# Performance work log

Measured on AMD Instinct MI355X. Metric: run time of the kernel, lower is better.

The kernel has to match this reference:

```python
import jax, jax.numpy as jnp
import numpy as np

KEY_SIZE = 256
EPS = 1e-8  # torch F.cosine_similarity default eps


def setup_inputs() -> dict:
    key = jax.random.key(0)
    k1, k2 = jax.random.split(key)
    B, M, K, V = 2048, 100000, KEY_SIZE, 256
    query = jax.random.normal(k1, (B, K), dtype=jnp.float32)
    memory = jax.random.normal(k2, (M, K + V), dtype=jnp.float32)
    return {"query": query, "memory": memory}


def reference(query, memory):
    # memory: [M, K+V] -> keys [M, K], values [M, V]
    keys = memory[:, :KEY_SIZE]
    values = memory[:, KEY_SIZE:]
    # cosine similarity: (q . k) / max(|q|*|k|, eps)  -> [B, M]
    dots = jnp.einsum('bk,mk->bm', query, keys)
    qn = jnp.linalg.norm(query, axis=1)  # [B]
    kn = jnp.linalg.norm(keys, axis=1)   # [M]
    sims = dots / jnp.maximum(qn[:, None] * kn[None, :], EPS)
    # top-1 over memory dim, then gather values -> [B, V]
    idx = jnp.argmax(sims, axis=1)
    return values[idx]
```

## Files before the change

kernel.cpp:

```cpp
#include <hip/hip_runtime.h>
#include <hip/hip_fp16.h>
#include <float.h>

#define MKEY 256
#define NMEM 100000
#define NPAD 100096
#define NQ   2048
#define BM 128
#define BN 128
#define NTILES 782
#define BLKPAD 800
#define GRID (128 * 98)
#define KEYBLOCKS (NPAD / 4)
#define QS (127.0f / 6.0f)
#define SS2 ((6.0f / 127.0f) * (6.0f / 127.0f))
#define GDELTA 0.04f
#define GINVD  25.0f

typedef int i32x4 __attribute__((ext_vector_type(4)));

__device__ inline void gll16(const void* g, void* l) {
  __builtin_amdgcn_global_load_lds(
      (const __attribute__((address_space(1))) unsigned*)g,
      (__attribute__((address_space(3))) unsigned*)l, 16, 0, 0);
}

__device__ inline int pack_i8x4(float4 v) {
  int c0 = max(-127, min(127, __float2int_rn(v.x * QS)));
  int c1 = max(-127, min(127, __float2int_rn(v.y * QS)));
  int c2 = max(-127, min(127, __float2int_rn(v.z * QS)));
  int c3 = max(-127, min(127, __float2int_rn(v.w * QS)));
  return (c0 & 255) | ((c1 & 255) << 8) | ((c2 & 255) << 16) | ((c3 & 255) << 24);
}

__device__ inline int dot4i8(int a, int b, int s) {
#if __has_builtin(__builtin_amdgcn_sdot4)
  return __builtin_amdgcn_sdot4(a, b, s, false);
#else
#pragma unroll
  for (int k = 0; k < 4; ++k) {
    const int av = (a << (24 - 8 * k)) >> 24;
    const int bv = (b << (24 - 8 * k)) >> 24;
    s += av * bv;
  }
  return s;
#endif
}

__global__ void convert(const float* __restrict__ q, const float* __restrict__ mem,
                        int* __restrict__ qi, int* __restrict__ ki,
                        float* __restrict__ rkn) {
  const int b = blockIdx.x;
  if (b >= KEYBLOCKS) {
    const int i = (b - KEYBLOCKS) * 256 + threadIdx.x;
    const float4 v = *(const float4*)&q[(size_t)i * 4];
    qi[i] = pack_i8x4(v);
    return;
  }
  const int t = threadIdx.x, lane = t & 63, w = t >> 6;
  const int row = b * 4 + w;
  if (row < NMEM) {
    const float4 v = *(const float4*)&mem[(long)row * 512 + lane * 4];
    const float ss0 = v.x * v.x + v.y * v.y + v.z * v.z + v.w * v.w;
    ki[(size_t)row * 64 + lane] = pack_i8x4(v);
    float ss = ss0;
#pragma unroll
    for (int off = 32; off >= 1; off >>= 1) ss += __shfl_xor(ss, off, 64);
    if (lane == 0) rkn[row] = 1.0f / sqrtf(fmaxf(ss, 1e-30f));
  } else {
    ki[(size_t)row * 64 + lane] = 0;
    if (lane == 0) rkn[row] = 0.f;
  }
}

__global__ __launch_bounds__(256, 4) void gemm_screen(
    const int* __restrict__ qi, const int* __restrict__ ki,
    const float* __restrict__ rkn,
    unsigned long long* __restrict__ bcode8, float* __restrict__ bmaxB) {
  __shared__ __align__(128) char smem[33792];

  const int id = blockIdx.x;
  const int mtile = (id >> 3) & 15;
  const int ntile = (id & 7) + 8 * (id >> 7);
  if (ntile >= NTILES) return;

  const int t = threadIdx.x;
  const int w = t >> 6;
  const int lane = t & 63;
  const int wr = w >> 1, wc = w & 1;
  const int q16 = lane >> 4, l16 = lane & 15;

  const int swz64 = ((lane & 3) ^ ((lane >> 2) & 3)) * 16;
  int soff4[4];
#pragma unroll
  for (int c = 0; c < 4; ++c)
    soff4[c] = ((w & 1) * 64 + c * 16 + (lane >> 2)) * 256 + swz64;
  const char* const asrc = (const char*)((w < 2) ? qi : ki) +
                           (size_t)(((w < 2) ? mtile : ntile) * 128) * 256;
  char* const dbase = smem + ((w < 2) ? 0 : 16384) + (w & 1) * 4096;

#define STG(p, s)                                         \
  do {                                                    \
    const char* _s = asrc + (s) * 64;                     \
    char* _d = dbase + (p) * 8192;                        \
    _Pragma("unroll")                                     \
    for (int c = 0; c < 4; ++c)                           \
      gll16(_s + soff4[c], _d + c * 1024);                \
  } while (0)

  i32x4 acc[4][4];
#pragma unroll
  for (int i = 0; i < 4; i++)
#pragma unroll
    for (int j = 0; j < 4; j++) acc[i][j] = (i32x4){0, 0, 0, 0};

  const int pc4 = (q16 ^ (l16 & 3)) * 16;

  STG(0, 0);
  __syncthreads();
#pragma unroll
  for (int s = 0; s < 4; ++s) {
    if (s < 3) STG((s + 1) & 1, s + 1);
    const int p = (s & 1) * 8192;
    i32x4 av[4], bv[4];
#pragma unroll
    for (int i = 0; i < 4; i++)
      av[i] = *(const i32x4*)&smem[p + (64 * wr + 16 * i + l16) * 64 + pc4];
#pragma unroll
    for (int j = 0; j < 4; j++)
      bv[j] = *(const i32x4*)&smem[16384 + p + (64 * wc + 16 * j + l16) * 64 + pc4];
#pragma unroll
    for (int i = 0; i < 4; i++)
#pragma unroll
      for (int j = 0; j < 4; j++)
        acc[i][j] = __builtin_amdgcn_mfma_i32_16x16x64_i8(av[i], bv[j], acc[i][j], 0, 0, 0);
    __syncthreads();
  }
#undef STG

  float rk[4];
#pragma unroll
  for (int j = 0; j < 4; j++) {
    const int ncol = ntile * BN + 64 * wc + 16 * j + l16;
    rk[j] = (ncol < NMEM) ? rkn[ncol] * SS2 : 0.f;
  }
  float (*L)[20] = (float(*)[20])smem;
  float* bhalf = (float*)(smem + 32768);
  const int wr_ = t >> 7, gg = (t >> 4) & 7, qrow = t & 15;
  float outv[4];
#pragma unroll
  for (int i = 0; i < 4; ++i) {
#pragma unroll
    for (int j = 0; j < 4; ++j)
#pragma unroll
      for (int r = 0; r < 4; ++r)
        L[(wr * 8 + wc * 4 + j) * 16 + q16 * 4 + r][l16] = (float)acc[i][j][r] * rk[j];
    __syncthreads();
    const float* Lr = L[(wr_ * 8 + gg) * 16 + qrow];
    const float4 a = *(const float4*)&Lr[0], b4 = *(const float4*)&Lr[4];
    const float4 cc = *(const float4*)&Lr[8], dd = *(const float4*)&Lr[12];
    float m = fmaxf(fmaxf(fmaxf(a.x, a.y), fmaxf(a.z, a.w)),
                    fmaxf(fmaxf(b4.x, b4.y), fmaxf(b4.z, b4.w)));
    m = fmaxf(m, fmaxf(fmaxf(cc.x, cc.y), fmaxf(cc.z, cc.w)));
    m = fmaxf(m, fmaxf(fmaxf(dd.x, dd.y), fmaxf(dd.z, dd.w)));
    outv[i] = m;
    float bm = fmaxf(m, __shfl_xor(m, 16, 64));
    bm = fmaxf(bm, __shfl_xor(bm, 32, 64));
    if (lane < 16) bhalf[(w * 16 + lane) * 4 + i] = bm;
    __syncthreads();
  }
  float* brow = (float*)smem;
  unsigned char* cb = (unsigned char*)(smem + 512);
  if (t < 128) {
    const int wrb = t >> 6, ib = (t >> 4) & 3, qr = t & 15;
    const float v = fmaxf(bhalf[((2 * wrb) * 16 + qr) * 4 + ib],
                          bhalf[((2 * wrb + 1) * 16 + qr) * 4 + ib]);
    brow[t] = v;
    bmaxB[(size_t)ntile * NQ + mtile * 128 + t] = v;
  }
  __syncthreads();
#pragma unroll
  for (int i = 0; i < 4; ++i) {
    const int row = wr_ * 64 + i * 16 + qrow;
    int code = (int)((brow[row] - outv[i]) * GINVD);
    code = min(255, max(0, code));
    cb[row * 8 + gg] = (unsigned char)code;
  }
  __syncthreads();
  if (t < 128)
    bcode8[(size_t)ntile * NQ + mtile * 128 + t] =
        *(const unsigned long long*)&cb[t * 8];
}

__global__ __launch_bounds__(256) void transpose_blk(const float* __restrict__ in,
                                                     float* __restrict__ outp) {
  __shared__ float tl[32][33];
  const int bid = blockIdx.x;
  const int ntt = bid % 25, qt = bid / 25;
  const int r0 = ntt * 32, c0 = qt * 32;
  const int tx = threadIdx.x & 31, ty = threadIdx.x >> 5;
#pragma unroll
  for (int k = 0; k < 4; ++k) {
    const int r = r0 + ty + 8 * k;
    tl[ty + 8 * k][tx] = (r < NTILES) ? in[(size_t)r * NQ + c0 + tx] : -FLT_MAX;
  }
  __syncthreads();
#pragma unroll
  for (int k = 0; k < 4; ++k) {
    const int qq = c0 + ty + 8 * k;
    const int nt = r0 + tx;
    if (nt < NTILES) outp[(size_t)qq * BLKPAD + nt] = tl[tx][ty + 8 * k];
  }
}

__global__ __launch_bounds__(256) void rescore_gather(
    const float* __restrict__ q, const float* __restrict__ mem,
    const int* __restrict__ qi8, const int* __restrict__ ki8,
    const float* __restrict__ rkn, const float* __restrict__ bmaxQ,
    const unsigned long long* __restrict__ bcode8, float* __restrict__ out) {
  __shared__ float red2[4];
  __shared__ int blist[64];
  __shared__ int nblk;
  __shared__ int glist[128];
  __shared__ int ng;
  __shared__ int rlist[256];
  __shared__ int nrow;
  __shared__ double wb[4];
  __shared__ int wbi[4];
  __shared__ int widx;

  const int qid = blockIdx.x;
  const int t = threadIdx.x, w = t >> 6, lane = t & 63;

  const float4 qv = *(const float4*)&q[(size_t)qid * 256 + lane * 4];
  float ss = qv.x * qv.x + qv.y * qv.y + qv.z * qv.z + qv.w * qv.w;
#pragma unroll
  for (int off = 32; off >= 1; off >>= 1) ss += __shfl_xor(ss, off, 64);
  const float qn = sqrtf(ss);
  const float margin = 1.8e-2f * qn;

  int4 qreg[4];
#pragma unroll
  for (int k = 0; k < 4; ++k)
    qreg[k] = *(const int4*)&qi8[(size_t)qid * 64 + (lane & 3) * 16 + k * 4];

  if (t == 0) { nblk = 0; ng = 0; nrow = 0; }
  const float* bq = &bmaxQ[(size_t)qid * BLKPAD];

  float gm = -FLT_MAX;
  for (int i = t; i < NTILES; i += 256) gm = fmaxf(gm, bq[i]);
#pragma unroll
  for (int off = 32; off >= 1; off >>= 1) gm = fmaxf(gm, __shfl_xor(gm, off, 64));
  if (lane == 0) red2[w] = gm;
  __syncthreads();
  gm = fmaxf(fmaxf(red2[0], red2[1]), fmaxf(red2[2], red2[3]));
  const float thresh = gm - margin;

  for (int i = t; i < NTILES; i += 256)
    if (bq[i] >= thresh) {
      int p = atomicAdd(&nblk, 1);
      if (p < 64) blist[p] = i;
    }
  __syncthreads();
  const int nb_ = min(nblk, 64);

  for (int idx = t; idx < nb_ * 8; idx += 256) {
    const int nt = blist[idx >> 3], gl = idx & 7;
    const unsigned long long cw = bcode8[(size_t)nt * NQ + qid];
    const int code = (int)((cw >> (8 * gl)) & 255);
    if ((float)code * GDELTA <= bq[nt] - thresh + 1e-6f) {
      int p = atomicAdd(&ng, 1);
      if (p < 128) glist[p] = nt * 8 + gl;
    }
  }
  __syncthreads();
  const int ng_ = min(ng, 128);

  for (int c = w; c < ng_; c += 4) {
    const int row = glist[c] * 16 + (lane >> 2);
    int idot = 0;
#pragma unroll
    for (int k = 0; k < 4; ++k) {
      const int4 kv = *(const int4*)&ki8[(size_t)row * 64 + (lane & 3) * 16 + k * 4];
      idot = dot4i8(kv.x, qreg[k].x, idot);
      idot = dot4i8(kv.y, qreg[k].y, idot);
      idot = dot4i8(kv.z, qreg[k].z, idot);
      idot = dot4i8(kv.w, qreg[k].w, idot);
    }
    idot += __shfl_xor(idot, 1, 64);
    idot += __shfl_xor(idot, 2, 64);
    if ((lane & 3) == 0 && row < NMEM) {
      const float sh = (float)idot * (rkn[row] * SS2);
      if (sh >= thresh) {
        int p = atomicAdd(&nrow, 1);
        if (p < 256) rlist[p] = row;
      }
    }
  }
  __syncthreads();
  const int nr = min(nrow, 256);

  double bestv = -1e300;
  int bestidx = 0x7fffffff;
  for (int c = w; c < nr; c += 4) {
    const int row = rlist[c];
    const float4 kv = *(const float4*)&mem[(size_t)row * 512 + lane * 4];
    double d = (double)kv.x * qv.x + (double)kv.y * qv.y +
               (double)kv.z * qv.z + (double)kv.w * qv.w;
    double s2 = (double)kv.x * kv.x + (double)kv.y * kv.y +
                (double)kv.z * kv.z + (double)kv.w * kv.w;
#pragma unroll
    for (int off = 32; off >= 1; off >>= 1) {
      d += __shfl_xor(d, off, 64);
      s2 += __shfl_xor(s2, off, 64);
    }
    if (lane == 0) {
      const double score = d / sqrt(s2 > 1e-300 ? s2 : 1e-300);
      if (score > bestv || (score == bestv && row < bestidx)) {
        bestv = score;
        bestidx = row;
      }
    }
  }
  if (lane == 0) { wb[w] = bestv; wbi[w] = bestidx; }
  __syncthreads();
  if (t == 0) {
    double bv = wb[0];
    int bi = wbi[0];
#pragma unroll
    for (int w2 = 1; w2 < 4; ++w2)
      if (wb[w2] > bv || (wb[w2] == bv && wbi[w2] < bi)) {
        bv = wb[w2];
        bi = wbi[w2];
      }
    widx = bi;
  }
  __syncthreads();
  out[(size_t)qid * 256 + t] = mem[(size_t)widx * 512 + 256 + t];
}

extern "C" void kernel_launch(void* const* d_in, const int* in_sizes, int n_in,
                              void* d_out, int out_size, void* d_ws, size_t ws_size,
                              hipStream_t stream) {
  const float* query = (const float*)d_in[0];
  const float* memory = (const float*)d_in[1];
  float* out = (float*)d_out;

  char* p = (char*)d_ws;
  int* qi = (int*)p; p += (size_t)NQ * 64 * 4;
  int* ki = (int*)p; p += (size_t)NPAD * 64 * 4;
  float* rkn = (float*)p; p += (size_t)NPAD * 4;
  float* bmaxB = (float*)p; p += (size_t)NTILES * NQ * 4;
  float* bmaxQ = (float*)p; p += (size_t)NQ * BLKPAD * 4;
  unsigned long long* bcode8 = (unsigned long long*)p;
  p += (size_t)NTILES * NQ * 8;

  hipLaunchKernelGGL(convert, dim3(KEYBLOCKS + NQ * MKEY / 1024), dim3(256), 0, stream,
                     query, memory, qi, ki, rkn);
  hipLaunchKernelGGL(gemm_screen, dim3(GRID), dim3(256), 0, stream,
                     qi, ki, rkn, bcode8, bmaxB);
  hipLaunchKernelGGL(transpose_blk, dim3(25 * 64), dim3(256), 0, stream, bmaxB, bmaxQ);
  hipLaunchKernelGGL(rescore_gather, dim3(NQ), dim3(256), 0, stream,
                     query, memory, qi, ki, rkn, bmaxQ, bcode8, out);
}
```

Baseline: 362.8 us.

## Use DPP row-max reductions in screen epilogue and widen convert per-thread work

The gemm_screen epilogue now reduces each 16-column group with DPP row_shr max operations in registers, replacing the staging of the full accumulator tile through LDS with multiple barriers. Only per-group maxima go to a small LDS array, and a single pass computes the block max and byte codes. The convert kernel now processes 16 rows per block, with each thread loading 64 bytes and storing an int4, which cuts the shuffle-reduction depth. LDS use drops slightly. The DPP reduction adds ALU work per accumulator element, and only 1 of 16 lanes writes to LDS.

```diff
diff --git a/kernel.cpp b/kernel.cpp
--- a/kernel.cpp
+++ b/kernel.cpp
@@ -11,7 +11,7 @@
 #define NTILES 782
 #define BLKPAD 800
 #define GRID (128 * 98)
-#define KEYBLOCKS (NPAD / 4)
+#define KB16 (NPAD / 16)
 #define QS (127.0f / 6.0f)
 #define SS2 ((6.0f / 127.0f) * (6.0f / 127.0f))
 #define GDELTA 0.04f
@@ -47,29 +47,50 @@
 #endif
 }
 
+__device__ inline float rowmax16(float x) {
+  int y;
+  y = __builtin_amdgcn_update_dpp(0, __float_as_int(x), 0x121, 0xF, 0xF, true);
+  x = fmaxf(x, __int_as_float(y));
+  y = __builtin_amdgcn_update_dpp(0, __float_as_int(x), 0x122, 0xF, 0xF, true);
+  x = fmaxf(x, __int_as_float(y));
+  y = __builtin_amdgcn_update_dpp(0, __float_as_int(x), 0x124, 0xF, 0xF, true);
+  x = fmaxf(x, __int_as_float(y));
+  y = __builtin_amdgcn_update_dpp(0, __float_as_int(x), 0x128, 0xF, 0xF, true);
+  return fmaxf(x, __int_as_float(y));
+}
+
 __global__ void convert(const float* __restrict__ q, const float* __restrict__ mem,
                         int* __restrict__ qi, int* __restrict__ ki,
                         float* __restrict__ rkn) {
-  const int b = blockIdx.x;
-  if (b >= KEYBLOCKS) {
-    const int i = (b - KEYBLOCKS) * 256 + threadIdx.x;
+  const int b = blockIdx.x, t = threadIdx.x;
+  if (b >= KB16) {
+    const int i = (b - KB16) * 256 + t;
     const float4 v = *(const float4*)&q[(size_t)i * 4];
     qi[i] = pack_i8x4(v);
     return;
   }
-  const int t = threadIdx.x, lane = t & 63, w = t >> 6;
-  const int row = b * 4 + w;
+  const int row = b * 16 + (t >> 4);
+  const int c = t & 15;
   if (row < NMEM) {
-    const float4 v = *(const float4*)&mem[(long)row * 512 + lane * 4];
-    const float ss0 = v.x * v.x + v.y * v.y + v.z * v.z + v.w * v.w;
-    ki[(size_t)row * 64 + lane] = pack_i8x4(v);
-    float ss = ss0;
-#pragma unroll
-    for (int off = 32; off >= 1; off >>= 1) ss += __shfl_xor(ss, off, 64);
-    if (lane == 0) rkn[row] = 1.0f / sqrtf(fmaxf(ss, 1e-30f));
+    const float* src = &mem[(size_t)row * 512 + c * 16];
+    const float4 v0 = *(const float4*)&src[0];
+    const float4 v1 = *(const float4*)&src[4];
+    const float4 v2 = *(const float4*)&src[8];
+    const float4 v3 = *(const float4*)&src[12];
+    float ss = v0.x * v0.x + v0.y * v0.y + v0.z * v0.z + v0.w * v0.w +
+               v1.x * v1.x + v1.y * v1.y + v1.z * v1.z + v1.w * v1.w +
+               v2.x * v2.x + v2.y * v2.y + v2.z * v2.z + v2.w * v2.w +
+               v3.x * v3.x + v3.y * v3.y + v3.z * v3.z + v3.w * v3.w;
+#pragma unroll
+    for (int off = 8; off >= 1; off >>= 1) ss += __shfl_xor(ss, off, 64);
+    int4 pk;
+    pk.x = pack_i8x4(v0); pk.y = pack_i8x4(v1);
+    pk.z = pack_i8x4(v2); pk.w = pack_i8x4(v3);
+    *(int4*)&ki[(size_t)row * 64 + c * 4] = pk;
+    if (c == 0) rkn[row] = 1.0f / sqrtf(fmaxf(ss, 1e-30f));
   } else {
-    ki[(size_t)row * 64 + lane] = 0;
-    if (lane == 0) rkn[row] = 0.f;
+    *(int4*)&ki[(size_t)row * 64 + c * 4] = make_int4(0, 0, 0, 0);
+    if (c == 0) rkn[row] = 0.f;
   }
 }
 
@@ -77,7 +98,7 @@
     const int* __restrict__ qi, const int* __restrict__ ki,
     const float* __restrict__ rkn,
     unsigned long long* __restrict__ bcode8, float* __restrict__ bmaxB) {
-  __shared__ __align__(128) char smem[33792];
+  __shared__ __align__(128) char smem[32768];
 
   const int id = blockIdx.x;
   const int mtile = (id >> 3) & 15;
@@ -144,52 +165,34 @@
     const int ncol = ntile * BN + 64 * wc + 16 * j + l16;
     rk[j] = (ncol < NMEM) ? rkn[ncol] * SS2 : 0.f;
   }
-  float (*L)[20] = (float(*)[20])smem;
-  float* bhalf = (float*)(smem + 32768);
-  const int wr_ = t >> 7, gg = (t >> 4) & 7, qrow = t & 15;
-  float outv[4];
-#pragma unroll
-  for (int i = 0; i < 4; ++i) {
+  float (*cg)[132] = (float(*)[132])smem;
+#pragma unroll
+  for (int i = 0; i < 4; ++i)
 #pragma unroll
     for (int j = 0; j < 4; ++j)
 #pragma unroll
-      for (int r = 0; r < 4; ++r)
-        L[(wr * 8 + wc * 4 + j) * 16 + q16 * 4 + r][l16] = (float)acc[i][j][r] * rk[j];
-    __syncthreads();
-    const float* Lr = L[(wr_ * 8 + gg) * 16 + qrow];
-    const float4 a = *(const float4*)&Lr[0], b4 = *(const float4*)&Lr[4];
-    const float4 cc = *(const float4*)&Lr[8], dd = *(const float4*)&Lr[12];
-    float m = fmaxf(fmaxf(fmaxf(a.x, a.y), fmaxf(a.z, a.w)),
-                    fmaxf(fmaxf(b4.x, b4.y), fmaxf(b4.z, b4.w)));
-    m = fmaxf(m, fmaxf(fmaxf(cc.x, cc.y), fmaxf(cc.z, cc.w)));
-    m = fmaxf(m, fmaxf(fmaxf(dd.x, dd.y), fmaxf(dd.z, dd.w)));
-    outv[i] = m;
-    float bm = fmaxf(m, __shfl_xor(m, 16, 64));
-    bm = fmaxf(bm, __shfl_xor(bm, 32, 64));
-    if (lane < 16) bhalf[(w * 16 + lane) * 4 + i] = bm;
-    __syncthreads();
-  }
-  float* brow = (float*)smem;
-  unsigned char* cb = (unsigned char*)(smem + 512);
+      for (int r = 0; r < 4; ++r) {
+        const float m = rowmax16((float)acc[i][j][r] * rk[j]);
+        if (l16 == 0)
+          cg[wc * 4 + j][64 * wr + 16 * i + 4 * q16 + r] = m;
+      }
+  __syncthreads();
   if (t < 128) {
-    const int wrb = t >> 6, ib = (t >> 4) & 3, qr = t & 15;
-    const float v = fmaxf(bhalf[((2 * wrb) * 16 + qr) * 4 + ib],
-                          bhalf[((2 * wrb + 1) * 16 + qr) * 4 + ib]);
-    brow[t] = v;
-    bmaxB[(size_t)ntile * NQ + mtile * 128 + t] = v;
-  }
-  __syncthreads();
-#pragma unroll
-  for (int i = 0; i < 4; ++i) {
-    const int row = wr_ * 64 + i * 16 + qrow;
-    int code = (int)((brow[row] - outv[i]) * GINVD);
-    code = min(255, max(0, code));
-    cb[row * 8 + gg] = (unsigned char)code;
-  }
-  __syncthreads();
-  if (t < 128)
-    bcode8[(size_t)ntile * NQ + mtile * 128 + t] =
-        *(const unsigned long long*)&cb[t * 8];
+    float v[8];
+#pragma unroll
+    for (int g = 0; g < 8; ++g) v[g] = cg[g][t];
+    float bm = fmaxf(fmaxf(fmaxf(v[0], v[1]), fmaxf(v[2], v[3])),
+                     fmaxf(fmaxf(v[4], v[5]), fmaxf(v[6], v[7])));
+    bmaxB[(size_t)ntile * NQ + mtile * 128 + t] = bm;
+    unsigned long long cw = 0;
+#pragma unroll
+    for (int g = 0; g < 8; ++g) {
+      int code = (int)((bm - v[g]) * GINVD);
+      code = min(255, max(0, code));
+      cw |= (unsigned long long)(unsigned)code << (8 * g);
+    }
+    bcode8[(size_t)ntile * NQ + mtile * 128 + t] = cw;
+  }
 }
 
 __global__ __launch_bounds__(256) void transpose_blk(const float* __restrict__ in,
@@ -355,7 +358,7 @@
   unsigned long long* bcode8 = (unsigned long long*)p;
   p += (size_t)NTILES * NQ * 8;
 
-  hipLaunchKernelGGL(convert, dim3(KEYBLOCKS + NQ * MKEY / 1024), dim3(256), 0, stream,
+  hipLaunchKernelGGL(convert, dim3(KB16 + NQ * MKEY / 1024), dim3(256), 0, stream,
                      query, memory, qi, ki, rkn);
   hipLaunchKernelGGL(gemm_screen, dim3(GRID), dim3(256), 0, stream,
                      qi, ki, rkn, bcode8, bmaxB);
```

New measurement: 388.9 us. 1.07x slower.
